# Kernel tuning notes

Hardware: AMD Instinct MI355X
Metric: run time of the kernel (lower is better)

Reference implementation:

```python
import math
import jax, jax.numpy as jnp
import numpy as np

N_LAYER = 6
THETA = 2.0 ** 16
LN_EPS = 1e-5


def _ln(x):
    # LayerNorm over last dim, no affine (elementwise_affine=False)
    mu = x.mean(-1, keepdims=True)
    var = ((x - mu) ** 2).mean(-1, keepdims=True)
    return (x - mu) / jnp.sqrt(var + LN_EPS)


def _rope(phases, v):
    # phases: (T, N); v: (B, H, T, N)
    ph = (phases % 1.0) * (2.0 * math.pi)
    c, s = jnp.cos(ph), jnp.sin(ph)
    v2 = v.reshape(v.shape[:-1] + (-1, 2))
    v_rot = jnp.stack((-v2[..., 1], v2[..., 0]), axis=-1).reshape(v.shape)
    return v * c + v_rot * s


def setup_inputs() -> dict:
    key = jax.random.key(0)
    ks = jax.random.split(key, 6)
    B, T, D, nh, mult, V = 2, 512, 256, 4, 64, 256
    N = D * mult // nh  # 4096 neurons per head
    std = 0.02
    return {
        "input_ids": jax.random.randint(ks[0], (B, T), 0, V, dtype=jnp.int64),
        "embed_table": jax.random.normal(ks[1], (V, D), jnp.float32) * std,
        "encoder": jax.random.normal(ks[2], (nh, D, N), jnp.float32) * std,
        "encoder_v": jax.random.normal(ks[3], (nh, D, N), jnp.float32) * std,
        "decoder": jax.random.normal(ks[4], (nh * N, D), jnp.float32) * std,
        "lm_head": jax.random.normal(ks[5], (D, V), jnp.float32) * std,
    }


def reference(input_ids, embed_table, encoder, encoder_v, decoder, lm_head):
    B, T = input_ids.shape
    nh, D, N = encoder.shape
    # RoPE freqs: quantize(arange(N), 2) / N exponent (matches get_freqs)
    qidx = jnp.floor(jnp.arange(N, dtype=jnp.float32) / 2.0) * 2.0
    freqs = 1.0 / (THETA ** (qidx / N)) / (2.0 * math.pi)
    phases = jnp.arange(T, dtype=jnp.float32)[:, None] * freqs[None, :]  # (T, N)
    # strictly-lower causal mask (tril with diagonal=-1)
    causal = jnp.tril(jnp.ones((T, T), dtype=bool), k=-1)
    dec = decoder.reshape(nh, N, D)  # head-major, matches transpose(1,2).reshape

    x = _ln(embed_table[input_ids])[:, None]  # (B, 1, T, D)
    trace = None
    for _ in range(N_LAYER):  # shared (tied) weights across layers
        x_sparse = jax.nn.relu(jnp.einsum('bitd,hdn->bhtn', x, encoder))  # (B,H,T,N)
        qr = _rope(phases, x_sparse)
        scores = jnp.einsum('bhtn,bhsn->bhts', qr, qr)  # linear attn, no softmax
        scores = jnp.where(causal, scores, 0.0)
        ykv = _ln(jnp.einsum('bhts,bisd->bhtd', scores, x))  # (B,H,T,D)
        y_sparse = jax.nn.relu(jnp.einsum('bhtd,hdn->bhtn', ykv, encoder_v))
        xy_sparse = x_sparse * y_sparse  # elementwise gate
        trace = xy_sparse  # keep only last layer (used for neuron_trace)
        ymlp = jnp.einsum('bhtn,hnd->btd', xy_sparse, dec)[:, None]  # (B,1,T,D)
        x = _ln(x + _ln(ymlp))

    xs = x[:, 0]  # (B, T, D)
    logits = xs @ lm_head  # (B, T, V)
    embedding = xs.mean(axis=1)  # (B, D), pool_output, no mask
    neuron_trace = trace.mean(axis=2).reshape(B, -1)  # (B, H*N)
    return logits, embedding, neuron_trace
```

## Files before the change

kernel.cpp:

```cpp
#include <hip/hip_runtime.h>
#include <hip/hip_bf16.h>
#include <hip/hip_fp16.h>

#define TT 512
#define DD 256
#define NH 4
#define NN 4096
#define VV 256
#define NLAYER 6
#define BB 2
#define BH (BB * NH)
#define NPAIR 2048

typedef __attribute__((ext_vector_type(8))) short bf16x8;
typedef __attribute__((ext_vector_type(4))) float f32x4;
typedef __attribute__((ext_vector_type(8))) unsigned short us8;
typedef __attribute__((ext_vector_type(4))) unsigned short us4;

#define AS1 __attribute__((address_space(1)))
#define AS3 __attribute__((address_space(3)))

__device__ __forceinline__ void glds16(const unsigned short* g, unsigned short* l) {
  __builtin_amdgcn_global_load_lds((const AS1 void*)g, (AS3 void*)l, 16, 0, 0);
}

__device__ __forceinline__ unsigned short f2bf(float f) {
  unsigned int u = __float_as_uint(f);
  return (unsigned short)((u + 0x7FFFu + ((u >> 16) & 1u)) >> 16);
}
__device__ __forceinline__ float bf2f(unsigned short h) {
  return __uint_as_float((unsigned int)h << 16);
}
__device__ __forceinline__ float h2f(unsigned short h) {
  __half x = *reinterpret_cast<__half*>(&h);
  return __half2float(x);
}

__device__ __forceinline__ float block_sum_256(float v) {
  __shared__ float s[4];
  #pragma unroll
  for (int o = 32; o > 0; o >>= 1) v += __shfl_down(v, o);
  int lane = threadIdx.x & 63, wid = threadIdx.x >> 6;
  if (lane == 0) s[wid] = v;
  __syncthreads();
  float r = s[0] + s[1] + s[2] + s[3];
  __syncthreads();
  return r;
}

__device__ __forceinline__ float wave_sum64(float v) {
  #pragma unroll
  for (int o = 32; o > 0; o >>= 1) v += __shfl_xor(v, o);
  return v;
}

__device__ __forceinline__ void mfma_tile128_w32_dbuf(const unsigned short* __restrict__ A, int lda,
                                                      const unsigned short* __restrict__ B, int ldb,
                                                      int K, f32x4 acc[2][8],
                                                      unsigned short* As, unsigned short* Bs) {
  const int tid = threadIdx.x;
  const int lane = tid & 63, wave = tid >> 6;
  const int fm = lane & 15, fq = lane >> 4;
  const int wrow = wave << 5;
  const int lrow = lane >> 3;
  const int scol = (((lane & 7) ^ lrow) << 3);
  const unsigned short* gA = A + (size_t)(wave * 8 + lrow) * lda + scol;
  const unsigned short* gB = B + (size_t)(wave * 8 + lrow) * ldb + scol;
  const int lbase = wave * 512;
  const int swz = (fm & 7) << 4;
  #pragma unroll
  for (int i = 0; i < 4; ++i) {
    glds16(gA + (size_t)(i * 32) * lda, As + lbase + i * 2048);
    glds16(gB + (size_t)(i * 32) * ldb, Bs + lbase + i * 2048);
  }
  __syncthreads();
  int cur = 0;
  for (int k0 = 0; k0 < K; k0 += 64) {
    if (k0 + 64 < K) {
      unsigned short* nA = As + (cur ^ 1) * 8192 + lbase;
      unsigned short* nB = Bs + (cur ^ 1) * 8192 + lbase;
      #pragma unroll
      for (int i = 0; i < 4; ++i) {
        glds16(gA + (k0 + 64) + (size_t)(i * 32) * lda, nA + i * 2048);
        glds16(gB + (k0 + 64) + (size_t)(i * 32) * ldb, nB + i * 2048);
      }
    }
    const char* cA = (const char*)(As + cur * 8192);
    const char* cB = (const char*)(Bs + cur * 8192);
    #pragma unroll
    for (int kk = 0; kk < 2; ++kk) {
      bf16x8 af[2], bfv[8];
      #pragma unroll
      for (int i = 0; i < 2; ++i) {
        const int ra = wrow + i * 16 + fm;
        af[i] = *(const bf16x8*)(cA + ((((ra << 7) + (kk << 6) + (fq << 4))) ^ swz));
      }
      #pragma unroll
      for (int i = 0; i < 8; ++i) {
        const int rb = i * 16 + fm;
        bfv[i] = *(const bf16x8*)(cB + ((((rb << 7) + (kk << 6) + (fq << 4))) ^ swz));
      }
      #pragma unroll
      for (int mi = 0; mi < 2; ++mi)
        #pragma unroll
        for (int ni = 0; ni < 8; ++ni)
          acc[mi][ni] = __builtin_amdgcn_mfma_f32_16x16x32_bf16(af[mi], bfv[ni], acc[mi][ni], 0, 0, 0);
    }
    __syncthreads();
    cur ^= 1;
  }
}

__device__ __forceinline__ void mfma_tile128_dbuf(const unsigned short* __restrict__ A, int lda,
                                                  const unsigned short* __restrict__ B, int ldb,
                                                  int K, f32x4 acc[4][4],
                                                  unsigned short* As, unsigned short* Bs) {
  const int tid = threadIdx.x;
  const int lane = tid & 63, wave = tid >> 6;
  const int fm = lane & 15, fq = lane >> 4;
  const int rw = (wave >> 1) << 6, cw = (wave & 1) << 6;
  const int lrow = lane >> 3;
  const int scol = (((lane & 7) ^ lrow) << 3);
  const unsigned short* gA = A + (size_t)(wave * 8 + lrow) * lda + scol;
  const unsigned short* gB = B + (size_t)(wave * 8 + lrow) * ldb + scol;
  const int lbase = wave * 512;
  const int swz = (fm & 7) << 4;
  #pragma unroll
  for (int i = 0; i < 4; ++i) {
    glds16(gA + (size_t)(i * 32) * lda, As + lbase + i * 2048);
    glds16(gB + (size_t)(i * 32) * ldb, Bs + lbase + i * 2048);
  }
  __syncthreads();
  int cur = 0;
  for (int k0 = 0; k0 < K; k0 += 64) {
    if (k0 + 64 < K) {
      unsigned short* nA = As + (cur ^ 1) * 8192 + lbase;
      unsigned short* nB = Bs + (cur ^ 1) * 8192 + lbase;
      #pragma unroll
      for (int i = 0; i < 4; ++i) {
        glds16(gA + (k0 + 64) + (size_t)(i * 32) * lda, nA + i * 2048);
        glds16(gB + (k0 + 64) + (size_t)(i * 32) * ldb, nB + i * 2048);
      }
    }
    const char* cA = (const char*)(As + cur * 8192);
    const char* cB = (const char*)(Bs + cur * 8192);
    #pragma unroll
    for (int kk = 0; kk < 2; ++kk) {
      bf16x8 af[4], bfv[4];
      #pragma unroll
      for (int i = 0; i < 4; ++i) {
        const int ra = rw + i * 16 + fm;
        const int rb = cw + i * 16 + fm;
        af[i]  = *(const bf16x8*)(cA + ((((ra << 7) + (kk << 6) + (fq << 4))) ^ swz));
        bfv[i] = *(const bf16x8*)(cB + ((((rb << 7) + (kk << 6) + (fq << 4))) ^ swz));
      }
      #pragma unroll
      for (int mi = 0; mi < 4; ++mi)
        #pragma unroll
        for (int ni = 0; ni < 4; ++ni)
          acc[mi][ni] = __builtin_amdgcn_mfma_f32_16x16x32_bf16(af[mi], bfv[ni], acc[mi][ni], 0, 0, 0);
    }
    __syncthreads();
    cur ^= 1;
  }
}


__global__ __launch_bounds__(256) void k_csinit(unsigned int* __restrict__ cs) {
  int idx = blockIdx.x * 256 + threadIdx.x;
  int t = idx >> 11, p = idx & (NPAIR - 1);
  const float INV2PI = 0.15915494309189535f;
  const float TWOPI = 6.283185307179586f;
  float f = exp2f(-16.0f * (float)(2 * p) / (float)NN) * INV2PI;
  float ph = fmodf((float)t * f, 1.0f) * TWOPI;
  float s, c;
  sincosf(ph, &s, &c);
  __half hc = __float2half_rn(c), hs = __float2half_rn(s);
  unsigned short uc = *reinterpret_cast<unsigned short*>(&hc);
  unsigned short us_ = *reinterpret_cast<unsigned short*>(&hs);
  cs[idx] = ((unsigned int)us_ << 16) | uc;
}

__global__ __launch_bounds__(256) void k_tcast3(const float* __restrict__ enc,
                                                const float* __restrict__ encv,
                                                const float* __restrict__ dec,
                                                unsigned short* __restrict__ encT,
                                                unsigned short* __restrict__ encvT,
                                                unsigned short* __restrict__ decT) {
  __shared__ float tile[64][65];
  const int lin = blockIdx.x;
  const float* in;
  unsigned short* out;
  int R, C, bx, by, bz;
  if (lin < 2048) {
    const int which = lin >> 10;
    in = which ? encv : enc; out = which ? encvT : encT; R = DD; C = NN;
    const int r = lin & 1023;
    bx = r & 63; by = (r >> 6) & 3; bz = r >> 8;
  } else {
    in = dec; out = decT; R = NN; C = DD;
    const int r = lin - 2048;
    bx = r & 3; by = (r >> 2) & 63; bz = r >> 8;
  }
  const size_t zoff = (size_t)bz * R * C;
  const int r0 = by * 64, c0 = bx * 64;
  const int cl = threadIdx.x & 63, r4 = threadIdx.x >> 6;
  #pragma unroll 4
  for (int i = 0; i < 16; ++i) {
    int rl = r4 * 16 + i;
    tile[rl][cl] = in[zoff + (size_t)(r0 + rl) * C + c0 + cl];
  }
  __syncthreads();
  #pragma unroll 4
  for (int i = 0; i < 16; ++i) {
    int ccl = r4 * 16 + i;
    out[zoff + (size_t)(c0 + ccl) * R + r0 + cl] = f2bf(tile[cl][ccl]);
  }
}

__global__ __launch_bounds__(256) void k_embed_ln(const int* __restrict__ idw,
                                                  const float* __restrict__ tbl,
                                                  float* __restrict__ x,
                                                  unsigned short* __restrict__ xbf,
                                                  unsigned short* __restrict__ xTbf) {
  __shared__ int s_id;
  int row = blockIdx.x, tid = threadIdx.x;
  if (tid == 0) {
    bool is64 = true;
    for (int i = 1; i < 64; i += 2)
      if (idw[i] != 0) { is64 = false; break; }
    s_id = is64 ? idw[2 * row] : idw[row];
  }
  __syncthreads();
  int id = s_id;
  float v = tbl[(size_t)id * DD + tid];
  float mu = block_sum_256(v) * (1.0f / DD);
  float d = v - mu;
  float var = block_sum_256(d * d) * (1.0f / DD);
  float r = d * rsqrtf(var + 1e-5f);
  x[(size_t)row * DD + tid] = r;
  unsigned short rb = f2bf(r);
  xbf[(size_t)row * DD + tid] = rb;
  int b = row >> 9, t = row & 511;
  xTbf[((size_t)b * DD + tid) * TT + t] = rb;
}


__global__ __launch_bounds__(256) void k_enc(const unsigned short* __restrict__ xbf,
                                             const unsigned short* __restrict__ encT,
                                             const unsigned int* __restrict__ csh,
                                             unsigned short* __restrict__ xsp,
                                             unsigned short* __restrict__ qr) {
  __shared__ unsigned short smem[32768];
  unsigned short* As = smem;
  unsigned short* Bs = smem + 16384;
  float* smemf = (float*)smem;
  const int tid = threadIdx.x;
  const int lin = blockIdx.x;
  const int bh = lin & 7, r0 = lin >> 3;
  const int b = bh >> 2, h = bh & 3;
  const int m0 = (r0 >> 5) * 128, n0 = (r0 & 31) * 128;
  f32x4 acc[2][8] = {};
  mfma_tile128_w32_dbuf(xbf + (size_t)b * TT * DD + (size_t)m0 * DD, DD,
                        encT + (size_t)h * NN * DD + (size_t)n0 * DD, DD, DD, acc, As, Bs);
  const int lane = tid & 63, wave = tid >> 6;
  const int fm = lane & 15, fq = lane >> 4;
  float* Scw = smemf + wave * (16 * 132);
  const int rr4 = lane >> 4, c0 = (lane & 15) << 3;
  const size_t base = (size_t)bh * TT * NN;
  #pragma unroll
  for (int mi = 0; mi < 2; ++mi) {
    if (mi) asm volatile("s_waitcnt lgkmcnt(0)" ::: "memory");
    #pragma unroll
    for (int ni = 0; ni < 8; ++ni)
      #pragma unroll
      for (int r = 0; r < 4; ++r)
        Scw[(fq * 4 + r) * 132 + ni * 16 + fm] = acc[mi][ni][r];
    asm volatile("s_waitcnt lgkmcnt(0)" ::: "memory");
    #pragma unroll
    for (int k = 0; k < 4; ++k) {
      const int rr = k * 4 + rr4;
      float v[8];
      *(float4*)&v[0] = *(const float4*)&Scw[rr * 132 + c0];
      *(float4*)&v[4] = *(const float4*)&Scw[rr * 132 + c0 + 4];
      const int t = m0 + wave * 32 + mi * 16 + rr;
      const int n = n0 + c0;
      #pragma unroll
      for (int j = 0; j < 8; ++j) v[j] = fmaxf(v[j], 0.0f);
      us8 o;
      #pragma unroll
      for (int j = 0; j < 8; ++j) o[j] = f2bf(v[j]);
      size_t off = base + (size_t)t * NN + n;
      *(us8*)(xsp + off) = o;
      const unsigned short* cp = (const unsigned short*)(csh + (size_t)t * NPAIR + (n >> 1));
      us8 cv = *(const us8*)cp;
      us8 q;
      #pragma unroll
      for (int j = 0; j < 4; ++j) {
        float c = h2f(cv[2 * j]), s = h2f(cv[2 * j + 1]);
        float ve = v[2 * j], vo = v[2 * j + 1];
        q[2 * j]     = f2bf(ve * c - vo * s);
        q[2 * j + 1] = f2bf(vo * c + ve * s);
      }
      *(us8*)(qr + off) = q;
    }
  }
}

__global__ __launch_bounds__(256) void k_scores_part(const unsigned short* __restrict__ qr,
                                                     float* __restrict__ scp) {
  __shared__ float smemf[16384];
  unsigned short* As = (unsigned short*)smemf;
  unsigned short* Bs = As + 16384;
  const int lin = blockIdx.x;
  const int xcd = lin & 7, slot = lin >> 3;
  const int zg = slot / 10, p = slot - zg * 10;
  const int z = xcd * 4 + zg;
  const int bh = z >> 2, kc = z & 3;
  const int mt = (p > 0) + (p > 2) + (p > 5);
  const int nt = p - mt * (mt + 1) / 2;
  const int m0 = mt * 128, n0 = nt * 128;
  const unsigned short* Q = qr + (size_t)bh * TT * NN + kc * 1024;
  f32x4 acc[4][4] = {};
  mfma_tile128_dbuf(Q + (size_t)m0 * NN, NN, Q + (size_t)n0 * NN, NN, 1024, acc, As, Bs);
  const int lane = threadIdx.x & 63, wave = threadIdx.x >> 6;
  const int fm = lane & 15, fq = lane >> 4;
  const int rw = (wave >> 1) << 6, cw = (wave & 1) << 6;
  float* C = scp + (size_t)z * TT * TT;
  const bool diag = (m0 == n0);
  #pragma unroll
  for (int ni = 0; ni < 4; ++ni) {
    int s = n0 + cw + ni * 16 + fm;
    #pragma unroll
    for (int mi = 0; mi < 4; ++mi) {
      int trow = m0 + rw + mi * 16 + (fq << 2);
      #pragma unroll
      for (int r = 0; r < 4; ++r) {
        float v = acc[mi][ni][r];
        if (diag && s >= trow + r) v = 0.0f;
        C[(size_t)(trow + r) * TT + s] = v;
      }
    }
  }
}

__global__ __launch_bounds__(256) void k_ykv_part(const float* __restrict__ scp,
                                                  const unsigned short* __restrict__ xTbf,
                                                  float* __restrict__ ykvp) {
  __shared__ unsigned short As[64][40];
  __shared__ unsigned short Bs[256][40];
  const int tid = threadIdx.x;
  const int lin = blockIdx.x;
  const int bh = lin & 7, r0 = lin >> 3;
  const int m0 = (r0 & 7) * 64, ks = r0 >> 3, b = bh >> 2;
  if (ks * 128 >= m0 + 64) return;
  float* C = ykvp + ((size_t)(bh * 4 + ks) * TT + m0) * DD;
  const int lane = tid & 63, wave = tid >> 6;
  const int srow = tid >> 2, sk = (tid & 3) << 3;
  const int fm = lane & 15, fq = lane >> 4;
  const int t = m0 + srow;
  const size_t abase0 = (size_t)(bh * 4) * TT * TT + (size_t)t * TT;
  const unsigned short* Brow = xTbf + ((size_t)b * DD + tid) * TT + ks * 128;
  f32x4 acc[16] = {};
  for (int k0 = 0; k0 < 128; k0 += 32) {
    const int s0 = ks * 128 + k0 + sk;
    const float* p = scp + abase0 + s0;
    float sum[8];
    float4 u0 = *(const float4*)(p);
    float4 u1 = *(const float4*)(p + 4);
    sum[0] = u0.x; sum[1] = u0.y; sum[2] = u0.z; sum[3] = u0.w;
    sum[4] = u1.x; sum[5] = u1.y; sum[6] = u1.z; sum[7] = u1.w;
    #pragma unroll
    for (int kc = 1; kc < 4; ++kc) {
      float4 v0 = *(const float4*)(p + (size_t)kc * TT * TT);
      float4 v1 = *(const float4*)(p + (size_t)kc * TT * TT + 4);
      sum[0] += v0.x; sum[1] += v0.y; sum[2] += v0.z; sum[3] += v0.w;
      sum[4] += v1.x; sum[5] += v1.y; sum[6] += v1.z; sum[7] += v1.w;
    }
    us8 av;
    #pragma unroll
    for (int j = 0; j < 8; ++j) av[j] = f2bf(sum[j]);
    us8 bv0 = *(const us8*)(Brow + k0);
    us8 bv1 = *(const us8*)(Brow + k0 + 8);
    us8 bv2 = *(const us8*)(Brow + k0 + 16);
    us8 bv3 = *(const us8*)(Brow + k0 + 24);
    __syncthreads();
    *(us8*)(&As[srow][sk]) = av;
    *(us8*)(&Bs[tid][0]) = bv0;
    *(us8*)(&Bs[tid][8]) = bv1;
    *(us8*)(&Bs[tid][16]) = bv2;
    *(us8*)(&Bs[tid][24]) = bv3;
    __syncthreads();
    bf16x8 a = *(const bf16x8*)(&As[wave * 16 + fm][fq << 3]);
    #pragma unroll
    for (int ni = 0; ni < 16; ++ni) {
      bf16x8 bfr = *(const bf16x8*)(&Bs[ni * 16 + fm][fq << 3]);
      acc[ni] = __builtin_amdgcn_mfma_f32_16x16x32_bf16(a, bfr, acc[ni], 0, 0, 0);
    }
  }
  const int trow = wave * 16 + (fq << 2);
  #pragma unroll
  for (int ni = 0; ni < 16; ++ni)
    #pragma unroll
    for (int r = 0; r < 4; ++r)
      C[(size_t)(trow + r) * DD + ni * 16 + fm] = acc[ni][r];
}

__global__ __launch_bounds__(256) void k_ykv_red(const float* __restrict__ ykvp,
                                                 unsigned short* __restrict__ ykvbf) {
  int row = blockIdx.x * 4 + (threadIdx.x >> 6);
  int lane = threadIdx.x & 63;
  int bh = row >> 9, t = row & 511;
  int d0 = lane << 2;
  int nks = (t >> 7) + 1;
  size_t base = ((size_t)(bh * 4) * TT + t) * DD + d0;
  f32x4 v = *(const f32x4*)(ykvp + base);
  if (nks > 1) v += *(const f32x4*)(ykvp + base + (size_t)TT * DD);
  if (nks > 2) v += *(const f32x4*)(ykvp + base + (size_t)2 * TT * DD);
  if (nks > 3) v += *(const f32x4*)(ykvp + base + (size_t)3 * TT * DD);
  float mu = wave_sum64(v.x + v.y + v.z + v.w) * (1.0f / DD);
  f32x4 d = v - mu;
  float var = wave_sum64(d.x * d.x + d.y * d.y + d.z * d.z + d.w * d.w) * (1.0f / DD);
  f32x4 r = d * rsqrtf(var + 1e-5f);
  us4 rb;
  #pragma unroll
  for (int j = 0; j < 4; ++j) rb[j] = f2bf(r[j]);
  *(us4*)(ykvbf + (size_t)row * DD + d0) = rb;
}

__global__ __launch_bounds__(256) void k_ysp_xy(const unsigned short* __restrict__ ykvbf,
                                                const unsigned short* __restrict__ encvT,
                                                const unsigned short* __restrict__ xsp,
                                                unsigned short* __restrict__ xy) {
  __shared__ unsigned short smem[32768];
  unsigned short* As = smem;
  unsigned short* Bs = smem + 16384;
  float* smemf = (float*)smem;
  const int tid = threadIdx.x;
  const int lin = blockIdx.x;
  const int bh = lin & 7, r0 = lin >> 3;
  const int h = bh & 3;
  const int m0 = (r0 >> 5) * 128, n0 = (r0 & 31) * 128;
  f32x4 acc[2][8] = {};
  mfma_tile128_w32_dbuf(ykvbf + (size_t)bh * TT * DD + (size_t)m0 * DD, DD,
                        encvT + (size_t)h * NN * DD + (size_t)n0 * DD, DD, DD, acc, As, Bs);
  const int lane = tid & 63, wave = tid >> 6;
  const int fm = lane & 15, fq = lane >> 4;
  float* Scw = smemf + wave * (16 * 132);
  const int rr4 = lane >> 4, c0 = (lane & 15) << 3;
  const size_t base = (size_t)bh * TT * NN;
  #pragma unroll
  for (int mi = 0; mi < 2; ++mi) {
    if (mi) asm volatile("s_waitcnt lgkmcnt(0)" ::: "memory");
    #pragma unroll
    for (int ni = 0; ni < 8; ++ni)
      #pragma unroll
      for (int r = 0; r < 4; ++r)
        Scw[(fq * 4 + r) * 132 + ni * 16 + fm] = acc[mi][ni][r];
    asm volatile("s_waitcnt lgkmcnt(0)" ::: "memory");
    #pragma unroll
    for (int k = 0; k < 4; ++k) {
      const int rr = k * 4 + rr4;
      float v[8];
      *(float4*)&v[0] = *(const float4*)&Scw[rr * 132 + c0];
      *(float4*)&v[4] = *(const float4*)&Scw[rr * 132 + c0 + 4];
      const int t = m0 + wave * 32 + mi * 16 + rr;
      const int n = n0 + c0;
      size_t off = base + (size_t)t * NN + n;
      us8 x0 = *(const us8*)(xsp + off);
      us8 o;
      #pragma unroll
      for (int j = 0; j < 8; ++j)
        o[j] = f2bf(bf2f(x0[j]) * fmaxf(v[j], 0.0f));
      *(us8*)(xy + off) = o;
    }
  }
}

__global__ __launch_bounds__(256) void k_ymlp(const unsigned short* __restrict__ xy,
                                              const unsigned short* __restrict__ decT,
                                              float* __restrict__ ym32) {
  __shared__ float smemf[16384];
  unsigned short* As = (unsigned short*)smemf;
  unsigned short* Bs = As + 16384;
  const int lin = blockIdx.x;
  const int bh = lin & 7, r0 = lin >> 3;
  const int ks = r0 >> 3, tile = r0 & 7;
  const int z = bh * 4 + ks, h = bh & 3;
  const int m0 = (tile & 3) * 128, n0 = (tile >> 2) * 128;
  f32x4 acc[4][4] = {};
  mfma_tile128_dbuf(xy + (size_t)bh * TT * NN + (size_t)m0 * NN + ks * 1024, NN,
                    decT + (size_t)h * DD * NN + (size_t)n0 * NN + ks * 1024, NN,
                    1024, acc, As, Bs);
  const int lane = threadIdx.x & 63, wave = threadIdx.x >> 6;
  const int fm = lane & 15, fq = lane >> 4;
  const int rw = (wave >> 1) << 6, cw = (wave & 1) << 6;
  float* C = ym32 + (size_t)z * TT * DD;
  #pragma unroll
  for (int ni = 0; ni < 4; ++ni) {
    int d = n0 + cw + ni * 16 + fm;
    #pragma unroll
    for (int mi = 0; mi < 4; ++mi) {
      int trow = m0 + rw + mi * 16 + (fq << 2);
      #pragma unroll
      for (int r = 0; r < 4; ++r)
        C[(size_t)(trow + r) * DD + d] = acc[mi][ni][r];
    }
  }
}

__global__ __launch_bounds__(256) void k_ln2(float* __restrict__ x,
                                             const float* __restrict__ ym32,
                                             unsigned short* __restrict__ xbf,
                                             unsigned short* __restrict__ xTbf) {
  int row = blockIdx.x * 4 + (threadIdx.x >> 6);
  int lane = threadIdx.x & 63;
  int b = row >> 9, t = row & 511;
  int d0 = lane << 2;
  f32x4 y = {0.0f, 0.0f, 0.0f, 0.0f};
  size_t rbase = (size_t)t * DD + d0;
  #pragma unroll
  for (int p = 0; p < 16; ++p)
    y += *(const f32x4*)(ym32 + (size_t)(b * 16 + p) * TT * DD + rbase);
  float mu = wave_sum64(y.x + y.y + y.z + y.w) * (1.0f / DD);
  f32x4 d = y - mu;
  float var = wave_sum64(d.x * d.x + d.y * d.y + d.z * d.z + d.w * d.w) * (1.0f / DD);
  f32x4 ly = d * rsqrtf(var + 1e-5f);
  f32x4 xv = *(const f32x4*)(x + (size_t)row * DD + d0) + ly;
  float mu2 = wave_sum64(xv.x + xv.y + xv.z + xv.w) * (1.0f / DD);
  f32x4 d2 = xv - mu2;
  float var2 = wave_sum64(d2.x * d2.x + d2.y * d2.y + d2.z * d2.z + d2.w * d2.w) * (1.0f / DD);
  f32x4 r = d2 * rsqrtf(var2 + 1e-5f);
  *(f32x4*)(x + (size_t)row * DD + d0) = r;
  us4 rb;
  #pragma unroll
  for (int j = 0; j < 4; ++j) rb[j] = f2bf(r[j]);
  *(us4*)(xbf + (size_t)row * DD + d0) = rb;
  #pragma unroll
  for (int j = 0; j < 4; ++j)
    xTbf[((size_t)b * DD + d0 + j) * TT + t] = rb[j];
}

__global__ __launch_bounds__(256) void k_trace_part(const unsigned short* __restrict__ xy,
                                                    float* __restrict__ part) {
  const int lin = blockIdx.x;
  const int ts = lin & 15, nc = (lin >> 4) & 1, bh = lin >> 5;
  const int n0 = nc * 2048 + threadIdx.x * 8;
  const size_t base = (size_t)bh * TT * NN + n0;
  float acc[8];
  #pragma unroll
  for (int j = 0; j < 8; ++j) acc[j] = 0.0f;
  for (int t = ts * 32; t < ts * 32 + 32; ++t) {
    us8 v = *(const us8*)(xy + base + (size_t)t * NN);
    #pragma unroll
    for (int j = 0; j < 8; ++j) acc[j] += bf2f(v[j]);
  }
  float* o = part + (size_t)(bh * 16 + ts) * NN + n0;
  #pragma unroll
  for (int j = 0; j < 8; ++j) o[j] = acc[j];
}

__global__ __launch_bounds__(256) void k_trace_red(const float* __restrict__ part,
                                                   float* __restrict__ out) {
  int idx = blockIdx.x * 256 + threadIdx.x;
  int bh = idx >> 12, n = idx & 4095;
  float s = 0.0f;
  #pragma unroll
  for (int ts = 0; ts < 16; ++ts)
    s += part[(size_t)(bh * 16 + ts) * NN + n];
  out[idx] = s * (1.0f / TT);
}

__global__ __launch_bounds__(256) void k_logits(const float* __restrict__ x,
                                                const float* __restrict__ W,
                                                float* __restrict__ out) {
  __shared__ float xs[DD];
  int row = blockIdx.x, tid = threadIdx.x;
  xs[tid] = x[(size_t)row * DD + tid];
  __syncthreads();
  float s = 0.0f;
  #pragma unroll 8
  for (int d = 0; d < DD; ++d) s = fmaf(xs[d], W[(size_t)d * VV + tid], s);
  out[(size_t)row * VV + tid] = s;
}

__global__ __launch_bounds__(256) void k_embed_part(const float* __restrict__ x,
                                                    float* __restrict__ part) {
  const int lin = blockIdx.x;
  const int tc = lin & 31, b = lin >> 5;
  const int d = threadIdx.x;
  float s = 0.0f;
  #pragma unroll
  for (int i = 0; i < 16; ++i)
    s += x[(size_t)(b * TT + tc * 16 + i) * DD + d];
  part[(size_t)lin * DD + d] = s;
}

__global__ __launch_bounds__(256) void k_embed_red(const float* __restrict__ part,
                                                   float* __restrict__ out) {
  int idx = blockIdx.x * 256 + threadIdx.x;
  int b = idx >> 8, d = idx & 255;
  float s = 0.0f;
  #pragma unroll
  for (int tc = 0; tc < 32; ++tc)
    s += part[(size_t)(b * 32 + tc) * DD + d];
  out[idx] = s * (1.0f / TT);
}

extern "C" void kernel_launch(void* const* d_in, const int* in_sizes, int n_in,
                              void* d_out, int out_size, void* d_ws, size_t ws_size,
                              hipStream_t stream) {
  const int*   ids  = (const int*)d_in[0];
  const float* tbl  = (const float*)d_in[1];
  const float* enc  = (const float*)d_in[2];
  const float* encv = (const float*)d_in[3];
  const float* dec  = (const float*)d_in[4];
  const float* lmh  = (const float*)d_in[5];

  float* ws   = (float*)d_ws;
  float* x    = ws;
  unsigned short* ykvbf = (unsigned short*)(x + 262144);
  float* ym32 = (float*)(ykvbf + 1048576);
  unsigned short* xbf   = (unsigned short*)(ym32 + 8388608);
  unsigned short* xTbf  = xbf + 262144;
  unsigned short* encT  = xTbf + 262144;
  unsigned short* encvT = encT + 4194304;
  unsigned short* decT  = encvT + 4194304;
  unsigned short* xspbf = decT + 4194304;
  unsigned short* qxybf = xspbf + 16777216;
  unsigned int* cs = (unsigned int*)(qxybf + 16777216);
  float* scp  = (float*)(cs + 2097152);
  float* ykvp = scp + 8388608;
  float* tpart = scp;
  float* epart = scp + 524288;

  float* out_logits = (float*)d_out;
  float* out_embed  = out_logits + (size_t)BB * TT * VV;
  float* out_trace  = out_embed + (size_t)BB * DD;

  k_csinit<<<(TT * NPAIR) / 256, 256, 0, stream>>>(cs);
  k_tcast3<<<3072, 256, 0, stream>>>(enc, encv, dec, encT, encvT, decT);

  k_embed_ln<<<BB * TT, 256, 0, stream>>>(ids, tbl, x, xbf, xTbf);
  for (int l = 0; l < NLAYER; ++l) {
    k_enc        <<<1024, 256, 0, stream>>>(xbf, encT, cs, xspbf, qxybf);
    k_scores_part<<<320, 256, 0, stream>>>(qxybf, scp);
    k_ykv_part   <<<256, 256, 0, stream>>>(scp, xTbf, ykvp);
    k_ykv_red    <<<BH * TT / 4, 256, 0, stream>>>(ykvp, ykvbf);
    k_ysp_xy     <<<1024, 256, 0, stream>>>(ykvbf, encvT, xspbf, qxybf);
    k_ymlp       <<<256, 256, 0, stream>>>(qxybf, decT, ym32);
    k_ln2        <<<BB * TT / 4, 256, 0, stream>>>(x, ym32, xbf, xTbf);
  }
  k_trace_part<<<256, 256, 0, stream>>>(qxybf, tpart);
  k_trace_red <<<128, 256, 0, stream>>>(tpart, out_trace);
  k_logits    <<<BB * TT, 256, 0, stream>>>(x, lmh, out_logits);
  k_embed_part<<<64, 256, 0, stream>>>(x, epart);
  k_embed_red <<<2, 256, 0, stream>>>(epart, out_embed);
}
```

Measured before the change: 704.7 us.

## Fuse ykv split-K reduction and LayerNorm into partial kernel via atomic tile counters

```diff
diff --git a/kernel.cpp b/kernel.cpp
--- a/kernel.cpp
+++ b/kernel.cpp
@@ -166,8 +166,10 @@
 }
 
 
-__global__ __launch_bounds__(256) void k_csinit(unsigned int* __restrict__ cs) {
+__global__ __launch_bounds__(256) void k_csinit(unsigned int* __restrict__ cs,
+                                                int* __restrict__ cnt) {
   int idx = blockIdx.x * 256 + threadIdx.x;
+  if (idx < 64) cnt[idx] = 0;
   int t = idx >> 11, p = idx & (NPAIR - 1);
   const float INV2PI = 0.15915494309189535f;
   const float TWOPI = 6.283185307179586f;
@@ -346,14 +348,22 @@
 
 __global__ __launch_bounds__(256) void k_ykv_part(const float* __restrict__ scp,
                                                   const unsigned short* __restrict__ xTbf,
-                                                  float* __restrict__ ykvp) {
+                                                  float* __restrict__ ykvp,
+                                                  unsigned short* __restrict__ ykvbf,
+                                                  int* __restrict__ cnt) {
   __shared__ unsigned short As[64][40];
   __shared__ unsigned short Bs[256][40];
+  __shared__ int s_old;
   const int tid = threadIdx.x;
   const int lin = blockIdx.x;
-  const int bh = lin & 7, r0 = lin >> 3;
-  const int m0 = (r0 & 7) * 64, ks = r0 >> 3, b = bh >> 2;
-  if (ks * 128 >= m0 + 64) return;
+  const int bh = lin & 7, p = lin >> 3;
+  int jp, ks;
+  if (p < 2)       { jp = p;                ks = 0; }
+  else if (p < 6)  { jp = 2 + ((p - 2) >> 1); ks = (p - 2) & 1; }
+  else if (p < 12) { jp = 4 + (p - 6) / 3;  ks = (p - 6) % 3; }
+  else             { jp = 6 + ((p - 12) >> 2); ks = (p - 12) & 3; }
+  const int m0 = jp * 64, b = bh >> 2;
+  const int need = (jp >> 1) + 1;
   float* C = ykvp + ((size_t)(bh * 4 + ks) * TT + m0) * DD;
   const int lane = tid & 63, wave = tid >> 6;
   const int srow = tid >> 2, sk = (tid & 3) << 3;
@@ -364,16 +374,16 @@
   f32x4 acc[16] = {};
   for (int k0 = 0; k0 < 128; k0 += 32) {
     const int s0 = ks * 128 + k0 + sk;
-    const float* p = scp + abase0 + s0;
+    const float* pp = scp + abase0 + s0;
     float sum[8];
-    float4 u0 = *(const float4*)(p);
-    float4 u1 = *(const float4*)(p + 4);
+    float4 u0 = *(const float4*)(pp);
+    float4 u1 = *(const float4*)(pp + 4);
     sum[0] = u0.x; sum[1] = u0.y; sum[2] = u0.z; sum[3] = u0.w;
     sum[4] = u1.x; sum[5] = u1.y; sum[6] = u1.z; sum[7] = u1.w;
     #pragma unroll
     for (int kc = 1; kc < 4; ++kc) {
-      float4 v0 = *(const float4*)(p + (size_t)kc * TT * TT);
-      float4 v1 = *(const float4*)(p + (size_t)kc * TT * TT + 4);
+      float4 v0 = *(const float4*)(pp + (size_t)kc * TT * TT);
+      float4 v1 = *(const float4*)(pp + (size_t)kc * TT * TT + 4);
       sum[0] += v0.x; sum[1] += v0.y; sum[2] += v0.z; sum[3] += v0.w;
       sum[4] += v1.x; sum[5] += v1.y; sum[6] += v1.z; sum[7] += v1.w;
     }
@@ -404,28 +414,31 @@
     #pragma unroll
     for (int r = 0; r < 4; ++r)
       C[(size_t)(trow + r) * DD + ni * 16 + fm] = acc[ni][r];
-}
-
-__global__ __launch_bounds__(256) void k_ykv_red(const float* __restrict__ ykvp,
-                                                 unsigned short* __restrict__ ykvbf) {
-  int row = blockIdx.x * 4 + (threadIdx.x >> 6);
-  int lane = threadIdx.x & 63;
-  int bh = row >> 9, t = row & 511;
-  int d0 = lane << 2;
-  int nks = (t >> 7) + 1;
-  size_t base = ((size_t)(bh * 4) * TT + t) * DD + d0;
-  f32x4 v = *(const f32x4*)(ykvp + base);
-  if (nks > 1) v += *(const f32x4*)(ykvp + base + (size_t)TT * DD);
-  if (nks > 2) v += *(const f32x4*)(ykvp + base + (size_t)2 * TT * DD);
-  if (nks > 3) v += *(const f32x4*)(ykvp + base + (size_t)3 * TT * DD);
-  float mu = wave_sum64(v.x + v.y + v.z + v.w) * (1.0f / DD);
-  f32x4 d = v - mu;
-  float var = wave_sum64(d.x * d.x + d.y * d.y + d.z * d.z + d.w * d.w) * (1.0f / DD);
-  f32x4 r = d * rsqrtf(var + 1e-5f);
-  us4 rb;
-  #pragma unroll
-  for (int j = 0; j < 4; ++j) rb[j] = f2bf(r[j]);
-  *(us4*)(ykvbf + (size_t)row * DD + d0) = rb;
+  __threadfence();
+  __syncthreads();
+  const int tile = bh * 8 + jp;
+  if (tid == 0) s_old = atomicAdd(&cnt[tile], 1);
+  __syncthreads();
+  if (s_old != need - 1) return;
+  __threadfence();
+  if (tid == 0) cnt[tile] = 0;
+  const int d0 = lane << 2;
+  for (int it = 0; it < 16; ++it) {
+    const int t2 = m0 + it * 4 + wave;
+    const size_t base2 = ((size_t)(bh * 4) * TT + t2) * DD + d0;
+    f32x4 v = *(const f32x4*)(ykvp + base2);
+    if (need > 1) v += *(const f32x4*)(ykvp + base2 + (size_t)TT * DD);
+    if (need > 2) v += *(const f32x4*)(ykvp + base2 + (size_t)2 * TT * DD);
+    if (need > 3) v += *(const f32x4*)(ykvp + base2 + (size_t)3 * TT * DD);
+    float mu = wave_sum64(v.x + v.y + v.z + v.w) * (1.0f / DD);
+    f32x4 d = v - mu;
+    float var = wave_sum64(d.x * d.x + d.y * d.y + d.z * d.z + d.w * d.w) * (1.0f / DD);
+    f32x4 r = d * rsqrtf(var + 1e-5f);
+    us4 rb;
+    #pragma unroll
+    for (int j = 0; j < 4; ++j) rb[j] = f2bf(r[j]);
+    *(us4*)(ykvbf + ((size_t)bh * TT + t2) * DD + d0) = rb;
+  }
 }
 
 __global__ __launch_bounds__(256) void k_ysp_xy(const unsigned short* __restrict__ ykvbf,
@@ -631,6 +644,7 @@
   unsigned int* cs = (unsigned int*)(qxybf + 16777216);
   float* scp  = (float*)(cs + 2097152);
   float* ykvp = scp + 8388608;
+  int*   cnt  = (int*)(ykvp + 4194304);
   float* tpart = scp;
   float* epart = scp + 524288;
 
@@ -638,15 +652,14 @@
   float* out_embed  = out_logits + (size_t)BB * TT * VV;
   float* out_trace  = out_embed + (size_t)BB * DD;
 
-  k_csinit<<<(TT * NPAIR) / 256, 256, 0, stream>>>(cs);
+  k_csinit<<<(TT * NPAIR) / 256, 256, 0, stream>>>(cs, cnt);
   k_tcast3<<<3072, 256, 0, stream>>>(enc, encv, dec, encT, encvT, decT);
 
   k_embed_ln<<<BB * TT, 256, 0, stream>>>(ids, tbl, x, xbf, xTbf);
   for (int l = 0; l < NLAYER; ++l) {
     k_enc        <<<1024, 256, 0, stream>>>(xbf, encT, cs, xspbf, qxybf);
     k_scores_part<<<320, 256, 0, stream>>>(qxybf, scp);
-    k_ykv_part   <<<256, 256, 0, stream>>>(scp, xTbf, ykvp);
-    k_ykv_red    <<<BH * TT / 4, 256, 0, stream>>>(ykvp, ykvbf);
+    k_ykv_part   <<<160, 256, 0, stream>>>(scp, xTbf, ykvp, ykvbf, cnt);
     k_ysp_xy     <<<1024, 256, 0, stream>>>(ykvbf, encvT, xspbf, qxybf);
     k_ymlp       <<<256, 256, 0, stream>>>(qxybf, decT, ym32);
     k_ln2        <<<BB * TT / 4, 256, 0, stream>>>(x, ym32, xbf, xTbf);
```

New measurement: 982.5 us. 1.39x slower.
